# Optimization experiments

Measured on AMD Instinct MI355X. Metric: run time of the kernel, lower is better.

Reference implementation:

```python
import jax, jax.numpy as jnp
import numpy as np

B, N, T, D = 8, 512, 24, 512
H, K = 8, 3
DK = D // H
PAD = (K - 1) // 2


def setup_inputs() -> dict:
    key = jax.random.key(0)
    ks = jax.random.split(key, 12)
    s_in = 1.0 / np.sqrt(D)
    s_conv = 1.0 / np.sqrt(D * K)
    inp = {
        "query": jax.random.normal(ks[0], (B, N, T, D), jnp.float32),
        "key": jax.random.normal(ks[1], (B, N, T, D), jnp.float32),
        "value": jax.random.normal(ks[2], (B, N, T, D), jnp.float32),
        # causal mask, shared structure across batch (torch code broadcasts it)
        "mask": jnp.broadcast_to(jnp.tril(jnp.ones((T, T), jnp.int32)), (B, T, T)),
        # Conv2d(d_model, d_model, (1, K)) weights, OIHW layout
        "Wq": jax.random.uniform(ks[3], (D, D, 1, K), jnp.float32, -s_conv, s_conv),
        "bq": jax.random.uniform(ks[4], (D,), jnp.float32, -s_conv, s_conv),
        "Wk": jax.random.uniform(ks[5], (D, D, 1, K), jnp.float32, -s_conv, s_conv),
        "bk": jax.random.uniform(ks[6], (D,), jnp.float32, -s_conv, s_conv),
        # Linear layers (weight stored as [out, in] like torch)
        "Wv": jax.random.uniform(ks[7], (D, D), jnp.float32, -s_in, s_in),
        "bv": jax.random.uniform(ks[8], (D,), jnp.float32, -s_in, s_in),
        "Wo": jax.random.uniform(ks[9], (D, D), jnp.float32, -s_in, s_in),
        "bo": jax.random.uniform(ks[10], (D,), jnp.float32, -s_in, s_in),
    }
    return inp


def _conv_proj(x, W, b):
    # x: (B, N, T, D) -> conv over T with kernel (1, K) -> (B, N, H, T, DK)
    xt = jnp.transpose(x, (0, 3, 1, 2))  # (B, D, N, T)
    y = jax.lax.conv_general_dilated(
        xt, W, window_strides=(1, 1), padding=((0, 0), (PAD, PAD)),
        dimension_numbers=("NCHW", "OIHW", "NCHW"))
    y = y + b[None, :, None, None]
    y = y.reshape(x.shape[0], H, DK, x.shape[1], x.shape[2])  # (B,H,DK,N,T)
    return jnp.transpose(y, (0, 3, 1, 4, 2))  # (B,N,H,T,DK)


def reference(query, key, value, mask, Wq, bq, Wk, bk, Wv, bv, Wo, bo):
    q = _conv_proj(query, Wq, bq)  # (B,N,H,T,DK)
    k = _conv_proj(key, Wk, bk)    # (B,N,H,T,DK)
    # value linear: (B,N,T,D) -> (B,N,H,T,DK)
    v = (jnp.einsum("bntd,ed->bnte", value, Wv) + bv)
    v = jnp.transpose(v.reshape(v.shape[0], v.shape[1], v.shape[2], H, DK), (0, 1, 3, 2, 4))
    scores = jnp.einsum("bnhtd,bnhsd->bnhts", q, k) / np.sqrt(DK)
    m = mask[:, None, None, :, :]  # (B,1,1,T,T)
    scores = jnp.where(m == 0, jnp.float32(-1e9), scores)
    p = jax.nn.softmax(scores, axis=-1)
    x = jnp.einsum("bnhts,bnhsd->bnhtd", p, v)
    x = jnp.transpose(x, (0, 1, 3, 2, 4)).reshape(x.shape[0], x.shape[1], T, H * DK)
    return jnp.einsum("bntd,ed->bnte", x, Wo) + bo
```

## Files before the change

### kernel.cpp

```cpp
#include <hip/hip_runtime.h>
#include <hip/hip_fp16.h>


typedef _Float16 f16x8 __attribute__((ext_vector_type(8)));
typedef float    f32x4 __attribute__((ext_vector_type(4)));

__device__ __forceinline__ void gload_lds16(const void* src, void* dst) {
    __builtin_amdgcn_global_load_lds(
        (const __attribute__((address_space(1))) void*)src,
        (__attribute__((address_space(3))) void*)dst, 16, 0, 0);
}

__global__ __launch_bounds__(512) void prep_weights(
    const float* __restrict__ Wq, const float* __restrict__ Wk,
    const float* __restrict__ Wv, const float* __restrict__ Wo,
    __half* __restrict__ Wq2, __half* __restrict__ Wk2,
    __half* __restrict__ Wv2, __half* __restrict__ Wo2)
{
    int i = blockIdx.x * 512 + threadIdx.x;
    if (i < 786432) {
        int o = i / 1536, r = i - o * 1536;
        int k = r >> 9, c = r & 511;
        int src = o * 1536 + c * 3 + k;
        Wq2[i] = __float2half(Wq[src]);
        Wk2[i] = __float2half(Wk[src]);
    } else {
        int j = i - 786432;
        Wv2[j] = __float2half(Wv[j]);
        Wo2[j] = __float2half(Wo[j]);
    }
}

template<int MODE, int KDIM, bool OUTF32>
__global__ __launch_bounds__(512, 4) void gemm_kernel(
    const void* __restrict__ Ap, const __half* __restrict__ Bw,
    const float* __restrict__ bias, void* __restrict__ Cp)
{
    __shared__ __half As[2][64 * 64];
    __shared__ __half Bs[2][256 * 64];

    const int tid  = threadIdx.x;
    const int lane = tid & 63;
    const int w    = tid >> 6;
    const int l15  = lane & 15, l4 = lane >> 4;
    const int mt   = blockIdx.x;
    const int nt   = blockIdx.y;

    const int rin  = lane >> 3;
    const int sfet = (lane & 7) ^ rin;

    const char* Bsrc = (const char*)Bw
        + ((size_t)(nt * 256 + w * 32) + rin) * (KDIM * 2)
        + (size_t)sfet * 16;
    const char* Asrc_lds = (const char*)Ap
        + ((size_t)(mt * 64 + w * 8) + rin) * (KDIM * 2)
        + (size_t)sfet * 16;

    const int arow  = tid >> 3;
    const int aslot = tid & 7;
    const int am    = mt * 64 + arow;
    const int abn   = am / 24;
    const int at    = am - abn * 24;
    const int assw  = aslot ^ (arow & 7);

    f32x4 acc[4][2] = {};
    float4 av0, av1;
    bool avalid = false;

    auto a_issue = [&](int kt) {
        const float* A = (const float*)Ap;
        const float* src;
        if (MODE == 0) {
            const int tap = kt >> 3;
            const int ib  = (kt & 7) << 6;
            const int ts  = at + tap - 1;
            avalid = ((unsigned)ts < 24u);
            src = avalid ? (A + ((size_t)abn * 24 + ts) * 512 + ib + (aslot << 3))
                         : A;
        } else {
            avalid = true;
            src = A + (size_t)am * 512 + (kt << 6) + (aslot << 3);
        }
        av0 = *(const float4*)src;
        av1 = *(const float4*)(src + 4);
    };
    auto a_write = [&](int buf) {
        union { _Float16 h[8]; uint4 u; } cv;
        if (avalid) {
            cv.h[0]=(_Float16)av0.x; cv.h[1]=(_Float16)av0.y;
            cv.h[2]=(_Float16)av0.z; cv.h[3]=(_Float16)av0.w;
            cv.h[4]=(_Float16)av1.x; cv.h[5]=(_Float16)av1.y;
            cv.h[6]=(_Float16)av1.z; cv.h[7]=(_Float16)av1.w;
        } else {
            #pragma unroll
            for (int q = 0; q < 8; ++q) cv.h[q] = (_Float16)0.f;
        }
        *(uint4*)((char*)As + buf * 8192 + arow * 128 + assw * 16) = cv.u;
    };
    auto stage_lds = [&](int buf, int kt) {
        if constexpr (MODE == 2) {
            gload_lds16(Asrc_lds + ((size_t)kt << 7),
                        (char*)As + buf * 8192 + w * 1024);
        }
        #pragma unroll
        for (int c = 0; c < 4; ++c) {
            gload_lds16(Bsrc + (size_t)c * (8 * KDIM * 2) + ((size_t)kt << 7),
                        (char*)Bs + buf * 32768 + (w * 4 + c) * 1024);
        }
    };

    constexpr int nsteps = KDIM >> 6;

    if constexpr (MODE != 2) { a_issue(0); a_write(0); }
    stage_lds(0, 0);
    __syncthreads();

    int cur = 0;
    for (int kt = 0; kt < nsteps; ++kt) {
        const bool hn = (kt + 1 < nsteps);
        if (hn) {
            if constexpr (MODE != 2) a_issue(kt + 1);
            stage_lds(cur ^ 1, kt + 1);
        }
        #pragma unroll
        for (int ks = 0; ks < 2; ++ks) {
            f16x8 af[4], bf[2];
            #pragma unroll
            for (int mi = 0; mi < 4; ++mi) {
                const int row = mi * 16 + l15;
                const int ss  = ((ks << 2) + l4) ^ (row & 7);
                af[mi] = *(const f16x8*)((const char*)As + cur * 8192
                                         + row * 128 + ss * 16);
            }
            #pragma unroll
            for (int ni = 0; ni < 2; ++ni) {
                const int row = w * 32 + ni * 16 + l15;
                const int ss  = ((ks << 2) + l4) ^ (row & 7);
                bf[ni] = *(const f16x8*)((const char*)Bs + cur * 32768
                                         + row * 128 + ss * 16);
            }
            #pragma unroll
            for (int mi = 0; mi < 4; ++mi)
                #pragma unroll
                for (int ni = 0; ni < 2; ++ni)
                    acc[mi][ni] = __builtin_amdgcn_mfma_f32_16x16x32_f16(
                        af[mi], bf[ni], acc[mi][ni], 0, 0, 0);
        }
        if (hn) { if constexpr (MODE != 2) a_write(cur ^ 1); }
        __syncthreads();
        cur ^= 1;
    }

    #pragma unroll
    for (int ni = 0; ni < 2; ++ni) {
        const int n = nt * 256 + w * 32 + ni * 16 + l15;
        const float bv = bias[n];
        #pragma unroll
        for (int mi = 0; mi < 4; ++mi) {
            #pragma unroll
            for (int j = 0; j < 4; ++j) {
                const size_t m = (size_t)mt * 64 + mi * 16 + l4 * 4 + j;
                const float v = acc[mi][ni][j] + bv;
                if (OUTF32) ((float*)Cp)[m * 512 + n] = v;
                else        ((__half*)Cp)[m * 512 + n] = __float2half(v);
            }
        }
    }
}

__global__ __launch_bounds__(256) void attn_kernel(
    const __half* __restrict__ Q, const __half* __restrict__ K,
    const __half* __restrict__ V, __half* __restrict__ X)
{
    __shared__ float smem[4 * 3864];
    const int tid = threadIdx.x, lane = tid & 63, w = tid >> 6;
    float* Qs = smem + w * 3864;
    float* Ks = Qs + 24 * 68;
    float* Ss = Ks + 24 * 68;

    const int unit = blockIdx.x * 4 + w;
    const int bn = unit >> 3, h = unit & 7;
    const size_t base = (size_t)bn * 24 * 512 + (size_t)h * 64;

    #pragma unroll
    for (int u = 0; u < 3; ++u) {
        const int idx = u * 64 + lane;
        const int r = idx >> 3, sl = idx & 7;
        f16x8 qv = *(const f16x8*)(Q + base + r * 512 + sl * 8);
        f16x8 kv = *(const f16x8*)(K + base + r * 512 + sl * 8);
        float4 q0 = { (float)qv[0], (float)qv[1], (float)qv[2], (float)qv[3] };
        float4 q1 = { (float)qv[4], (float)qv[5], (float)qv[6], (float)qv[7] };
        float4 k0 = { (float)kv[0], (float)kv[1], (float)kv[2], (float)kv[3] };
        float4 k1 = { (float)kv[4], (float)kv[5], (float)kv[6], (float)kv[7] };
        *(float4*)&Qs[r * 68 + sl * 8]     = q0;
        *(float4*)&Qs[r * 68 + sl * 8 + 4] = q1;
        *(float4*)&Ks[r * 68 + sl * 8]     = k0;
        *(float4*)&Ks[r * 68 + sl * 8 + 4] = k1;
    }
    float vcol[24];
    #pragma unroll
    for (int s = 0; s < 24; ++s)
        vcol[s] = __half2float(V[base + s * 512 + lane]);
    __syncthreads();

    #pragma unroll
    for (int it = 0; it < 9; ++it) {
        const int j = it * 64 + lane;
        const int t = j / 24, s = j - t * 24;
        float a = 0.f;
        #pragma unroll
        for (int e = 0; e < 64; e += 4) {
            float4 qv = *(const float4*)&Qs[t * 68 + e];
            float4 kv = *(const float4*)&Ks[s * 68 + e];
            a += qv.x * kv.x + qv.y * kv.y + qv.z * kv.z + qv.w * kv.w;
        }
        Ss[t * 25 + s] = a * 0.125f;
    }
    __syncthreads();

    if (lane < 24) {
        const int t = lane;
        float m = -1e30f;
        for (int s = 0; s <= t; ++s) m = fmaxf(m, Ss[t * 25 + s]);
        float sum = 0.f;
        for (int s = 0; s <= t; ++s) {
            float p = __expf(Ss[t * 25 + s] - m);
            sum += p;
            Ss[t * 25 + s] = p;
        }
        const float inv = 1.f / sum;
        for (int s = 0; s <= t; ++s) Ss[t * 25 + s] *= inv;
    }
    __syncthreads();

    #pragma unroll
    for (int t = 0; t < 24; ++t) {
        float a = 0.f;
        #pragma unroll
        for (int s = 0; s < 24; ++s) {
            if (s <= t) a += Ss[t * 25 + s] * vcol[s];
        }
        X[base + t * 512 + lane] = __float2half(a);
    }
}

extern "C" void kernel_launch(void* const* d_in, const int* in_sizes, int n_in,
                              void* d_out, int out_size, void* d_ws, size_t ws_size,
                              hipStream_t stream)
{
    const float* query = (const float*)d_in[0];
    const float* key   = (const float*)d_in[1];
    const float* value = (const float*)d_in[2];
    const float* Wq = (const float*)d_in[4];
    const float* bq = (const float*)d_in[5];
    const float* Wk = (const float*)d_in[6];
    const float* bk = (const float*)d_in[7];
    const float* Wv = (const float*)d_in[8];
    const float* bv = (const float*)d_in[9];
    const float* Wo = (const float*)d_in[10];
    const float* bo = (const float*)d_in[11];

    char* ws = (char*)d_ws;
    __half* Qb  = (__half*)ws;
    __half* Kb  = (__half*)(ws + 100663296);
    __half* Vb  = (__half*)(ws + 201326592);
    __half* Wq2 = (__half*)(ws + 301989888);
    __half* Wk2 = Wq2 + 786432;
    __half* Wv2 = Wk2 + 786432;
    __half* Wo2 = Wv2 + 262144;

    prep_weights<<<2048, 512, 0, stream>>>(Wq, Wk, Wv, Wo, Wq2, Wk2, Wv2, Wo2);

    gemm_kernel<0, 1536, false><<<dim3(1536, 2), 512, 0, stream>>>(query, Wq2, bq, Qb);
    gemm_kernel<0, 1536, false><<<dim3(1536, 2), 512, 0, stream>>>(key,   Wk2, bk, Kb);
    gemm_kernel<1,  512, false><<<dim3(1536, 2), 512, 0, stream>>>(value, Wv2, bv, Vb);

    attn_kernel<<<8192, 256, 0, stream>>>(Qb, Kb, Vb, Qb );

    gemm_kernel<2,  512, true><<<dim3(1536, 2), 512, 0, stream>>>(Qb, Wo2, bo, d_out);
}
```

Measured before the change: 1.356 ms.

## Pre-convert padded fp16 Q/K inputs and retile GEMMs to 128x128 blocks

Adds a conversion kernel that writes query and key as fp16 with zero time-padding rows. The conv-projection GEMMs can then stage A through direct global-to-LDS loads instead of converting per tile in registers. All GEMMs also switch from 64x256 tiles with 512 threads to 128x128 tiles with 256 threads and a 2x2 warp grid, which gives more balanced reuse of A and B. The trade is an extra full read and write pass over query and key, plus a larger workspace.

```diff
diff --git a/kernel.cpp b/kernel.cpp
--- a/kernel.cpp
+++ b/kernel.cpp
@@ -31,18 +31,47 @@
     }
 }
 
+__global__ __launch_bounds__(256) void convert_qk(
+    const float* __restrict__ q, const float* __restrict__ k,
+    __half* __restrict__ Qpad, __half* __restrict__ Kpad)
+{
+    const int id = blockIdx.x * 256 + threadIdx.x;
+    const bool isK = id >= 6815744;
+    const int u = isK ? id - 6815744 : id;
+    const float* __restrict__ src = isK ? k : q;
+    __half* __restrict__ dst = isK ? Kpad : Qpad;
+    const int bn  = u / 1664;
+    const int rem = u - bn * 1664;
+    const int tau = rem >> 6;
+    const int cs  = rem & 63;
+    union { _Float16 h[8]; uint4 uu; } cv;
+    if (tau >= 1 && tau <= 24) {
+        const float* p = src + ((size_t)bn * 24 + (tau - 1)) * 512 + cs * 8;
+        float4 a = *(const float4*)p, b = *(const float4*)(p + 4);
+        cv.h[0]=(_Float16)a.x; cv.h[1]=(_Float16)a.y;
+        cv.h[2]=(_Float16)a.z; cv.h[3]=(_Float16)a.w;
+        cv.h[4]=(_Float16)b.x; cv.h[5]=(_Float16)b.y;
+        cv.h[6]=(_Float16)b.z; cv.h[7]=(_Float16)b.w;
+    } else {
+        #pragma unroll
+        for (int j = 0; j < 8; ++j) cv.h[j] = (_Float16)0.f;
+    }
+    *(uint4*)(dst + (size_t)bn * 13312 + tau * 512 + cs * 8) = cv.uu;
+}
+
 template<int MODE, int KDIM, bool OUTF32>
-__global__ __launch_bounds__(512, 4) void gemm_kernel(
+__global__ __launch_bounds__(256, 2) void gemm_kernel(
     const void* __restrict__ Ap, const __half* __restrict__ Bw,
     const float* __restrict__ bias, void* __restrict__ Cp)
 {
-    __shared__ __half As[2][64 * 64];
-    __shared__ __half Bs[2][256 * 64];
+    __shared__ __half As[2][128 * 64];
+    __shared__ __half Bs[2][128 * 64];
 
     const int tid  = threadIdx.x;
     const int lane = tid & 63;
     const int w    = tid >> 6;
     const int l15  = lane & 15, l4 = lane >> 4;
+    const int wr   = w >> 1, wc = w & 1;
     const int mt   = blockIdx.x;
     const int nt   = blockIdx.y;
 
@@ -50,116 +79,122 @@
     const int sfet = (lane & 7) ^ rin;
 
     const char* Bsrc = (const char*)Bw
-        + ((size_t)(nt * 256 + w * 32) + rin) * (KDIM * 2)
-        + (size_t)sfet * 16;
-    const char* Asrc_lds = (const char*)Ap
-        + ((size_t)(mt * 64 + w * 8) + rin) * (KDIM * 2)
-        + (size_t)sfet * 16;
-
-    const int arow  = tid >> 3;
-    const int aslot = tid & 7;
-    const int am    = mt * 64 + arow;
-    const int abn   = am / 24;
-    const int at    = am - abn * 24;
-    const int assw  = aslot ^ (arow & 7);
-
-    f32x4 acc[4][2] = {};
-    float4 av0, av1;
-    bool avalid = false;
+        + ((size_t)(nt * 128) + rin) * (KDIM * 2) + (size_t)sfet * 16;
+
+    const char* Asrc[4];
+    if constexpr (MODE != 1) {
+        #pragma unroll
+        for (int c = 0; c < 4; ++c) {
+            const int arow = mt * 128 + (w * 4 + c) * 8 + rin;
+            if constexpr (MODE == 0) {
+                const int bn = arow / 24, at = arow - bn * 24;
+                Asrc[c] = (const char*)Ap + (size_t)bn * 26624
+                          + (size_t)at * 1024 + (size_t)sfet * 16;
+            } else {
+                Asrc[c] = (const char*)Ap + (size_t)arow * (KDIM * 2)
+                          + (size_t)sfet * 16;
+            }
+        }
+    }
+
+    f32x4 acc[4][4] = {};
+    float4 av[4][2];
 
     auto a_issue = [&](int kt) {
-        const float* A = (const float*)Ap;
-        const float* src;
-        if (MODE == 0) {
-            const int tap = kt >> 3;
-            const int ib  = (kt & 7) << 6;
-            const int ts  = at + tap - 1;
-            avalid = ((unsigned)ts < 24u);
-            src = avalid ? (A + ((size_t)abn * 24 + ts) * 512 + ib + (aslot << 3))
-                         : A;
-        } else {
-            avalid = true;
-            src = A + (size_t)am * 512 + (kt << 6) + (aslot << 3);
-        }
-        av0 = *(const float4*)src;
-        av1 = *(const float4*)(src + 4);
+        #pragma unroll
+        for (int u2 = 0; u2 < 4; ++u2) {
+            const int gu = tid + u2 * 256;
+            const int row = gu >> 3, slot = gu & 7;
+            const float* p = (const float*)Ap
+                + ((size_t)(mt * 128 + row)) * 512 + kt * 64 + slot * 8;
+            av[u2][0] = *(const float4*)p;
+            av[u2][1] = *(const float4*)(p + 4);
+        }
     };
     auto a_write = [&](int buf) {
-        union { _Float16 h[8]; uint4 u; } cv;
-        if (avalid) {
-            cv.h[0]=(_Float16)av0.x; cv.h[1]=(_Float16)av0.y;
-            cv.h[2]=(_Float16)av0.z; cv.h[3]=(_Float16)av0.w;
-            cv.h[4]=(_Float16)av1.x; cv.h[5]=(_Float16)av1.y;
-            cv.h[6]=(_Float16)av1.z; cv.h[7]=(_Float16)av1.w;
-        } else {
-            #pragma unroll
-            for (int q = 0; q < 8; ++q) cv.h[q] = (_Float16)0.f;
-        }
-        *(uint4*)((char*)As + buf * 8192 + arow * 128 + assw * 16) = cv.u;
+        #pragma unroll
+        for (int u2 = 0; u2 < 4; ++u2) {
+            const int gu = tid + u2 * 256;
+            const int row = gu >> 3, slot = gu & 7;
+            union { _Float16 h[8]; uint4 uu; } cv;
+            cv.h[0]=(_Float16)av[u2][0].x; cv.h[1]=(_Float16)av[u2][0].y;
+            cv.h[2]=(_Float16)av[u2][0].z; cv.h[3]=(_Float16)av[u2][0].w;
+            cv.h[4]=(_Float16)av[u2][1].x; cv.h[5]=(_Float16)av[u2][1].y;
+            cv.h[6]=(_Float16)av[u2][1].z; cv.h[7]=(_Float16)av[u2][1].w;
+            *(uint4*)((char*)&As[buf][0] + row * 128 + (slot ^ (row & 7)) * 16)
+                = cv.uu;
+        }
     };
-    auto stage_lds = [&](int buf, int kt) {
-        if constexpr (MODE == 2) {
-            gload_lds16(Asrc_lds + ((size_t)kt << 7),
-                        (char*)As + buf * 8192 + w * 1024);
-        }
-        #pragma unroll
-        for (int c = 0; c < 4; ++c) {
-            gload_lds16(Bsrc + (size_t)c * (8 * KDIM * 2) + ((size_t)kt << 7),
-                        (char*)Bs + buf * 32768 + (w * 4 + c) * 1024);
-        }
+    auto stage = [&](int buf, int kt) {
+        if constexpr (MODE != 1) {
+            const size_t koffA = (MODE == 0)
+                ? (size_t)(((kt >> 3) << 10) + ((kt & 7) << 7))
+                : (size_t)kt << 7;
+            #pragma unroll
+            for (int c = 0; c < 4; ++c)
+                gload_lds16(Asrc[c] + koffA,
+                            (char*)&As[buf][0] + (w * 4 + c) * 1024);
+        }
+        #pragma unroll
+        for (int c = 0; c < 4; ++c)
+            gload_lds16(Bsrc + (size_t)(w * 4 + c) * 8 * (KDIM * 2)
+                             + ((size_t)kt << 7),
+                        (char*)&Bs[buf][0] + (w * 4 + c) * 1024);
     };
+    auto compute = [&](int buf) {
+        #pragma unroll
+        for (int ks = 0; ks < 2; ++ks) {
+            f16x8 af[4], bf[4];
+            #pragma unroll
+            for (int mi = 0; mi < 4; ++mi) {
+                const int row = wr * 64 + mi * 16 + l15;
+                const int ss  = ((ks << 2) + l4) ^ (row & 7);
+                af[mi] = *(const f16x8*)((const char*)&As[buf][0]
+                                         + row * 128 + ss * 16);
+            }
+            #pragma unroll
+            for (int ni = 0; ni < 4; ++ni) {
+                const int row = wc * 64 + ni * 16 + l15;
+                const int ss  = ((ks << 2) + l4) ^ (row & 7);
+                bf[ni] = *(const f16x8*)((const char*)&Bs[buf][0]
+                                         + row * 128 + ss * 16);
+            }
+            #pragma unroll
+            for (int mi = 0; mi < 4; ++mi)
+                #pragma unroll
+                for (int ni = 0; ni < 4; ++ni)
+                    acc[mi][ni] = __builtin_amdgcn_mfma_f32_16x16x32_f16(
+                        af[mi], bf[ni], acc[mi][ni], 0, 0, 0);
+        }
+    };
 
     constexpr int nsteps = KDIM >> 6;
-
-    if constexpr (MODE != 2) { a_issue(0); a_write(0); }
-    stage_lds(0, 0);
+    if constexpr (MODE == 1) { a_issue(0); a_write(0); }
+    stage(0, 0);
     __syncthreads();
 
     int cur = 0;
     for (int kt = 0; kt < nsteps; ++kt) {
         const bool hn = (kt + 1 < nsteps);
         if (hn) {
-            if constexpr (MODE != 2) a_issue(kt + 1);
-            stage_lds(cur ^ 1, kt + 1);
-        }
-        #pragma unroll
-        for (int ks = 0; ks < 2; ++ks) {
-            f16x8 af[4], bf[2];
-            #pragma unroll
-            for (int mi = 0; mi < 4; ++mi) {
-                const int row = mi * 16 + l15;
-                const int ss  = ((ks << 2) + l4) ^ (row & 7);
-                af[mi] = *(const f16x8*)((const char*)As + cur * 8192
-                                         + row * 128 + ss * 16);
-            }
-            #pragma unroll
-            for (int ni = 0; ni < 2; ++ni) {
-                const int row = w * 32 + ni * 16 + l15;
-                const int ss  = ((ks << 2) + l4) ^ (row & 7);
-                bf[ni] = *(const f16x8*)((const char*)Bs + cur * 32768
-                                         + row * 128 + ss * 16);
-            }
-            #pragma unroll
-            for (int mi = 0; mi < 4; ++mi)
-                #pragma unroll
-                for (int ni = 0; ni < 2; ++ni)
-                    acc[mi][ni] = __builtin_amdgcn_mfma_f32_16x16x32_f16(
-                        af[mi], bf[ni], acc[mi][ni], 0, 0, 0);
-        }
-        if (hn) { if constexpr (MODE != 2) a_write(cur ^ 1); }
+            if constexpr (MODE == 1) a_issue(kt + 1);
+            stage(cur ^ 1, kt + 1);
+        }
+        compute(cur);
+        if (hn) { if constexpr (MODE == 1) a_write(cur ^ 1); }
         __syncthreads();
         cur ^= 1;
     }
 
     #pragma unroll
-    for (int ni = 0; ni < 2; ++ni) {
-        const int n = nt * 256 + w * 32 + ni * 16 + l15;
+    for (int ni = 0; ni < 4; ++ni) {
+        const int n = nt * 128 + wc * 64 + ni * 16 + l15;
         const float bv = bias[n];
         #pragma unroll
         for (int mi = 0; mi < 4; ++mi) {
             #pragma unroll
             for (int j = 0; j < 4; ++j) {
-                const size_t m = (size_t)mt * 64 + mi * 16 + l4 * 4 + j;
+                const size_t m = (size_t)mt * 128 + wr * 64 + mi * 16 + l4 * 4 + j;
                 const float v = acc[mi][ni][j] + bv;
                 if (OUTF32) ((float*)Cp)[m * 512 + n] = v;
                 else        ((__half*)Cp)[m * 512 + n] = __float2half(v);
@@ -261,21 +296,24 @@
     const float* bo = (const float*)d_in[11];
 
     char* ws = (char*)d_ws;
-    __half* Qb  = (__half*)ws;
-    __half* Kb  = (__half*)(ws + 100663296);
-    __half* Vb  = (__half*)(ws + 201326592);
-    __half* Wq2 = (__half*)(ws + 301989888);
-    __half* Wk2 = Wq2 + 786432;
-    __half* Wv2 = Wk2 + 786432;
-    __half* Wo2 = Wv2 + 262144;
+    __half* Qpad = (__half*)ws;
+    __half* Kpad = (__half*)(ws + 109051904);
+    __half* Qb   = (__half*)(ws + 218103808);
+    __half* Kb   = (__half*)(ws + 318767104);
+    __half* Vb   = (__half*)ws;
+    __half* Wq2  = (__half*)(ws + 419430400);
+    __half* Wk2  = Wq2 + 786432;
+    __half* Wv2  = Wk2 + 786432;
+    __half* Wo2  = Wv2 + 262144;
 
     prep_weights<<<2048, 512, 0, stream>>>(Wq, Wk, Wv, Wo, Wq2, Wk2, Wv2, Wo2);
-
-    gemm_kernel<0, 1536, false><<<dim3(1536, 2), 512, 0, stream>>>(query, Wq2, bq, Qb);
-    gemm_kernel<0, 1536, false><<<dim3(1536, 2), 512, 0, stream>>>(key,   Wk2, bk, Kb);
-    gemm_kernel<1,  512, false><<<dim3(1536, 2), 512, 0, stream>>>(value, Wv2, bv, Vb);
+    convert_qk<<<53248, 256, 0, stream>>>(query, key, Qpad, Kpad);
+
+    gemm_kernel<0, 1536, false><<<dim3(768, 4), 256, 0, stream>>>(Qpad, Wq2, bq, Qb);
+    gemm_kernel<0, 1536, false><<<dim3(768, 4), 256, 0, stream>>>(Kpad, Wk2, bk, Kb);
+    gemm_kernel<1,  512, false><<<dim3(768, 4), 256, 0, stream>>>(value, Wv2, bv, Vb);
 
     attn_kernel<<<8192, 256, 0, stream>>>(Qb, Kb, Vb, Qb );
 
-    gemm_kernel<2,  512, true><<<dim3(1536, 2), 512, 0, stream>>>(Qb, Wo2, bo, d_out);
-}
+    gemm_kernel<2,  512, true><<<dim3(768, 4), 256, 0, stream>>>(Qb, Wo2, bo, d_out);
+}
```

Result: slower. 1.424 ms (+5.0%).
